# Performance work log

Hardware: AMD Instinct MI355X
Metric: run time of the kernel (lower is better)

Reference implementation:

```python
import jax, jax.numpy as jnp
import numpy as np


def _gcn_layer(x, row, col, W, b):
    # x: [N, d_in]; row/col: [E'] (with self loops already appended)
    N = x.shape[0]
    deg = jax.ops.segment_sum(jnp.ones_like(row, dtype=x.dtype), row, num_segments=N)
    deg_inv_sqrt = deg ** -0.5  # self loops guarantee deg >= 1
    norm = deg_inv_sqrt[row] * deg_inv_sqrt[col]  # [E']
    msg = norm[:, None] * x[row]                  # gather + normalize
    aggr = jax.ops.segment_sum(msg, col, num_segments=N)  # scatter-add
    return aggr @ W + b


def reference(x, edge_index, W1, b1, W2, b2):
    N = x.shape[0]
    loops = jnp.arange(N, dtype=edge_index.dtype)
    row = jnp.concatenate([edge_index[0], loops])
    col = jnp.concatenate([edge_index[1], loops])
    h = jax.nn.relu(_gcn_layer(x, row, col, W1, b1))
    # F.dropout(training=self.training) is identity in eval mode
    out = _gcn_layer(h, row, col, W2, b2)
    return jax.nn.log_softmax(out, axis=1)


def setup_inputs() -> dict:
    key = jax.random.key(0)
    k1, k2, k3, k4 = jax.random.split(key, 4)
    N, E, F_IN, F_HID, F_OUT = 100000, 1200000, 64, 64, 16
    x = jax.random.normal(k1, (N, F_IN), dtype=jnp.float32)
    edge_index = jax.random.randint(k2, (2, E), 0, N, dtype=jnp.int64)
    W1 = jax.random.normal(k3, (F_IN, F_HID), dtype=jnp.float32) / np.sqrt(F_IN)
    b1 = jnp.zeros((F_HID,), dtype=jnp.float32)
    W2 = jax.random.normal(k4, (F_HID, F_OUT), dtype=jnp.float32) / np.sqrt(F_HID)
    b2 = jnp.zeros((F_OUT,), dtype=jnp.float32)
    return {"x": x, "edge_index": edge_index, "W1": W1, "b1": b1, "W2": W2, "b2": b2}
```

## Files before the change

### kernel.cpp

```cpp
#include <hip/hip_runtime.h>
#include <hip/hip_bf16.h>

typedef __attribute__((ext_vector_type(8))) _Float16 hfrag;
typedef __attribute__((ext_vector_type(4))) float ffrag;
typedef __attribute__((ext_vector_type(4))) _Float16 h4v;

#define BSH 8
#define LBS 256
#define CAP_SH 14
#define CAP (1 << CAP_SH)
#define CONV_BLKS 384
#define NF 128
#define NBKP 512

__device__ __forceinline__ float b2f_(unsigned short u) {
    return __uint_as_float(((unsigned)u) << 16);
}
__device__ __forceinline__ unsigned short f2b_(float v) {
    __hip_bfloat16 h = __float2bfloat16(v);
    return *reinterpret_cast<unsigned short*>(&h);
}
__device__ __forceinline__ unsigned short f2h_(float v) {
    _Float16 h = (_Float16)v;
    return __builtin_bit_cast(unsigned short, h);
}
__device__ __forceinline__ float h2f_(unsigned short u) {
    _Float16 h = __builtin_bit_cast(_Float16, u);
    return (float)h;
}

__device__ __forceinline__ float loadF(const void* p, long long i, int isF32) {
    if (isF32) return ((const float*)p)[i];
    return b2f_(((const unsigned short*)p)[i]);
}

__device__ __forceinline__ float4 loadF4(const void* p, long long base, int i4, int isF32) {
    if (isF32) {
        return ((const float4*)((const float*)p + base))[i4];
    } else {
        ushort4 u = ((const ushort4*)((const unsigned short*)p + base))[i4];
        return make_float4(b2f_(u.x), b2f_(u.y), b2f_(u.z), b2f_(u.w));
    }
}

__device__ __forceinline__ void get_edge(const int* ei, int i64, int e, int E, int& s, int& d) {
    if (i64) { s = ei[2 * (long long)e]; d = ei[2 * (long long)E + 2 * (long long)e]; }
    else     { s = ei[e];                d = ei[(long long)E + e]; }
}

struct E4 { int s[4]; int d[4]; };
__device__ __forceinline__ E4 load4(const int* __restrict__ ei, int i64, int e0, int E) {
    E4 r;
    if (i64) {
        const int4* ps = (const int4*)(ei + 2 * (long long)e0);
        const int4* pd = (const int4*)(ei + 2 * (long long)E + 2 * (long long)e0);
        int4 a = ps[0], b = ps[1];
        int4 c = pd[0], d = pd[1];
        r.s[0] = a.x; r.s[1] = a.z; r.s[2] = b.x; r.s[3] = b.z;
        r.d[0] = c.x; r.d[1] = c.z; r.d[2] = d.x; r.d[3] = d.z;
    } else {
        int4 a = *(const int4*)(ei + e0);
        int4 c = *(const int4*)(ei + (long long)E + e0);
        r.s[0] = a.x; r.s[1] = a.y; r.s[2] = a.z; r.s[3] = a.w;
        r.d[0] = c.x; r.d[1] = c.y; r.d[2] = c.z; r.d[3] = c.w;
    }
    return r;
}

__device__ __forceinline__ void wave_scan_excl(int* a, int nEl, int lane) {
    int run = 0;
    for (int base = 0; base < nEl; base += 64) {
        int i = base + lane;
        int orig = (i < nEl) ? a[i] : 0;
        int v = orig;
#pragma unroll
        for (int off = 1; off < 64; off <<= 1) {
            int u = __shfl_up(v, off);
            if (lane >= off) v += u;
        }
        if (i < nEl) a[i] = v - orig + run;
        run += __shfl(v, 63);
    }
}

__global__ void k_prep(const void* x, const int* ei,
                       const void* W1, const void* b1, const void* W2, const void* b2,
                       int* flags, float* Wbuf) {
    __shared__ int s_sane, s_zero;
    int tid = threadIdx.x;
    if (tid == 0) { s_sane = 0; s_zero = 0; }
    __syncthreads();
    const unsigned short* xu = (const unsigned short*)x;
    int sane = 0;
    for (int k = tid; k < 4096; k += 256) {
        float v = b2f_(xu[2 * k]);
        float a = fabsf(v);
        if (v == 0.0f || (a >= 9.3e-10f && a <= 1.1e9f)) sane++;
    }
    if (sane) atomicAdd(&s_sane, sane);
    int zero = 0;
    for (int k = tid; k < 1024; k += 256) if (ei[2 * k + 1] == 0) zero++;
    if (zero) atomicAdd(&s_zero, zero);
    __syncthreads();
    int f = (s_sane < 3000) ? 1 : 0;
    if (tid == 0) { flags[0] = f; flags[1] = (s_zero > 512) ? 1 : 0; }
    for (int i = tid; i < 4096; i += 256) Wbuf[i] = loadF(W1, i, f);
    if (tid < 64) Wbuf[4096 + tid] = loadF(b1, tid, f);
    for (int i = tid; i < 1024; i += 256) Wbuf[4160 + i] = loadF(W2, i, f);
    if (tid < 16) Wbuf[5184 + tid] = loadF(b2, tid, f);
}

__global__ __launch_bounds__(256) void k_s1(const void* __restrict__ x,
                                            const int* __restrict__ ei,
                                            const int* __restrict__ flags,
                                            int E, int N, int nbk,
                                            int* __restrict__ cnt_d, int* __restrict__ cnt_s,
                                            unsigned short* __restrict__ xh) {
    __shared__ int hd[512], hs[512];
    int tid = threadIdx.x;
    if (blockIdx.x < CONV_BLKS) {
        int f = flags[0];
        int n4 = N * 16;
        int ctid = blockIdx.x * 256 + tid;
        int stride = CONV_BLKS * 256 * 2;
        for (int i0 = ctid * 2; i0 < n4; i0 += stride) {
            float4 v0 = loadF4(x, 0, i0, f);
            float4 v1 = (i0 + 1 < n4) ? loadF4(x, 0, i0 + 1, f) : make_float4(0, 0, 0, 0);
            ushort4 o0, o1;
            o0.x = f2h_(v0.x); o0.y = f2h_(v0.y); o0.z = f2h_(v0.z); o0.w = f2h_(v0.w);
            o1.x = f2h_(v1.x); o1.y = f2h_(v1.y); o1.z = f2h_(v1.z); o1.w = f2h_(v1.w);
            ((ushort4*)xh)[i0] = o0;
            if (i0 + 1 < n4) ((ushort4*)xh)[i0 + 1] = o1;
        }
        return;
    }
    for (int i = tid; i < 512; i += 256) { hd[i] = 0; hs[i] = 0; }
    __syncthreads();
    int i64 = flags[1];
    int fb = blockIdx.x - CONV_BLKS;
    int ctid = fb * 256 + tid;
    int stride = NF * 256 * 8;
    for (int e0 = ctid * 8; e0 + 8 <= E; e0 += stride) {
        E4 a = load4(ei, i64, e0, E);
        E4 b = load4(ei, i64, e0 + 4, E);
#pragma unroll
        for (int u = 0; u < 4; ++u) {
            atomicAdd(&hd[a.d[u] >> BSH], 1);
            atomicAdd(&hs[a.s[u] >> BSH], 1);
            atomicAdd(&hd[b.d[u] >> BSH], 1);
            atomicAdd(&hs[b.s[u] >> BSH], 1);
        }
    }
    if (fb == 0 && tid == 0) {
        for (int e = E & ~7; e < E; ++e) {
            int s, d;
            get_edge(ei, i64, e, E, s, d);
            atomicAdd(&hd[d >> BSH], 1);
            atomicAdd(&hs[s >> BSH], 1);
        }
    }
    __syncthreads();
    for (int i = tid; i < nbk; i += 256) {
        cnt_d[fb * NBKP + i] = hd[i];
        cnt_s[fb * NBKP + i] = hs[i];
    }
}

__global__ __launch_bounds__(128) void k_s2(const int* __restrict__ cnt_d,
                                            const int* __restrict__ cnt_s,
                                            int nbk,
                                            int* __restrict__ base_d, int* __restrict__ base_s,
                                            int* __restrict__ td, int* __restrict__ ts) {
    __shared__ int vd[NF], vs[NF];
    __shared__ int lastd, lasts;
    int b = blockIdx.x, tid = threadIdx.x;
    for (int i = tid; i < NF; i += 128) { vd[i] = cnt_d[i * NBKP + b]; vs[i] = cnt_s[i * NBKP + b]; }
    __syncthreads();
    if (tid == 0) lastd = vd[NF - 1];
    if (tid == 1) lasts = vs[NF - 1];
    __syncthreads();
    int lane = tid & 63;
    if (tid < 64)       wave_scan_excl(vd, NF, lane);
    else if (tid < 128) wave_scan_excl(vs, NF, lane);
    __syncthreads();
    for (int i = tid; i < NF; i += 128) {
        base_d[i * NBKP + b] = (b << CAP_SH) + vd[i];
        base_s[i * NBKP + b] = (b << CAP_SH) + vs[i];
    }
    if (tid == 0) td[b] = (b << CAP_SH) + vd[NF - 1] + lastd;
    if (tid == 1) ts[b] = (b << CAP_SH) + vs[NF - 1] + lasts;
}

__global__ __launch_bounds__(256) void k_fill(const int* __restrict__ ei,
                                              const int* __restrict__ flags,
                                              int E, int nbk,
                                              const int* __restrict__ base_d,
                                              const int* __restrict__ base_s,
                                              int* __restrict__ pdst,
                                              unsigned char* __restrict__ psrc) {
    __shared__ int bd[512], bs[512];
    int tid = threadIdx.x;
    int fb = blockIdx.x;
    for (int i = tid; i < nbk; i += 256) {
        bd[i] = base_d[fb * NBKP + i];
        bs[i] = base_s[fb * NBKP + i];
    }
    __syncthreads();
    int i64 = flags[1];
    int ctid = fb * 256 + tid;
    int stride = NF * 256 * 8;
    for (int e0 = ctid * 8; e0 + 8 <= E; e0 += stride) {
        E4 a = load4(ei, i64, e0, E);
        E4 b = load4(ei, i64, e0 + 4, E);
#pragma unroll
        for (int u = 0; u < 4; ++u) {
            int db = a.d[u] >> BSH, sb = a.s[u] >> BSH;
            int p = atomicAdd(&bd[db], 1);
            if (p < ((db + 1) << CAP_SH)) pdst[p] = (a.s[u] << BSH) | (a.d[u] & (LBS - 1));
            int q = atomicAdd(&bs[sb], 1);
            if (q < ((sb + 1) << CAP_SH)) psrc[q] = (unsigned char)(a.s[u] & (LBS - 1));
            db = b.d[u] >> BSH; sb = b.s[u] >> BSH;
            p = atomicAdd(&bd[db], 1);
            if (p < ((db + 1) << CAP_SH)) pdst[p] = (b.s[u] << BSH) | (b.d[u] & (LBS - 1));
            q = atomicAdd(&bs[sb], 1);
            if (q < ((sb + 1) << CAP_SH)) psrc[q] = (unsigned char)(b.s[u] & (LBS - 1));
        }
    }
    if (fb == 0 && tid == 0) {
        for (int e = E & ~7; e < E; ++e) {
            int s, d;
            get_edge(ei, i64, e, E, s, d);
            int db = d >> BSH, sb = s >> BSH;
            int p = atomicAdd(&bd[db], 1);
            if (p < ((db + 1) << CAP_SH)) pdst[p] = (s << BSH) | (d & (LBS - 1));
            int q = atomicAdd(&bs[sb], 1);
            if (q < ((sb + 1) << CAP_SH)) psrc[q] = (unsigned char)(s & (LBS - 1));
        }
    }
}

__global__ __launch_bounds__(256) void k_deg(const unsigned char* __restrict__ psrc,
                                             const int* __restrict__ ts,
                                             float* __restrict__ dis, int N) {
    __shared__ int h[LBS];
    int b = blockIdx.x, tid = threadIdx.x;
    if (tid < LBS) h[tid] = 0;
    __syncthreads();
    int beg = b << CAP_SH;
    int end = min(ts[b], (b + 1) << CAP_SH);
    int cnt = end - beg;
    int nv = cnt & ~3;
    for (int off = 4 * tid; off < nv; off += 1024) {
        uchar4 v = *(const uchar4*)(psrc + beg + off);
        atomicAdd(&h[v.x], 1); atomicAdd(&h[v.y], 1);
        atomicAdd(&h[v.z], 1); atomicAdd(&h[v.w], 1);
    }
    if (tid < cnt - nv) atomicAdd(&h[psrc[beg + nv + tid]], 1);
    __syncthreads();
    if (tid < LBS) {
        int node = b * LBS + tid;
        if (node < N) dis[node] = rsqrtf((float)h[tid] + 1.0f);
    }
}

__global__ __launch_bounds__(256) void k_csr(const int* __restrict__ pdst,
                                             const int* __restrict__ td,
                                             const float* __restrict__ dis,
                                             int2* __restrict__ row_se,
                                             int2* __restrict__ pke, int N) {
    __shared__ int h[LBS], lb[LBS], cur[LBS];
    int b = blockIdx.x, tid = threadIdx.x;
    if (tid < LBS) h[tid] = 0;
    __syncthreads();
    int beg = b << CAP_SH;
    int end = min(td[b], (b + 1) << CAP_SH);
    for (int p = beg + tid; p < end; p += 256) atomicAdd(&h[pdst[p] & (LBS - 1)], 1);
    __syncthreads();
    if (tid < LBS) lb[tid] = h[tid];
    __syncthreads();
    if (tid < 64) wave_scan_excl(lb, LBS, tid);
    __syncthreads();
    if (tid < LBS) {
        cur[tid] = lb[tid];
        int node = b * LBS + tid;
        if (node < N) row_se[node] = make_int2(beg + lb[tid], beg + lb[tid] + h[tid]);
    }
    __syncthreads();
    for (int p = beg + tid; p < end; p += 256) {
        int e = pdst[p];
        int src = e >> BSH, ld = e & (LBS - 1);
        int r = atomicAdd(&cur[ld], 1);
        pke[beg + r] = make_int2(src, __float_as_int(dis[src]));
    }
}

__global__ __launch_bounds__(256) void k_agg(const unsigned short* __restrict__ xh,
                                             const float* __restrict__ dis,
                                             const int2* __restrict__ row_se,
                                             const int2* __restrict__ pke,
                                             unsigned short* __restrict__ aggb, int N) {
    int tid = threadIdx.x;
    int lane = tid & 63;
    int g = lane >> 4, i4 = lane & 15;
    int n = blockIdx.x * 16 + (tid >> 6) * 4 + g;
    if (n >= N) return;
    float dd = dis[n];
    int2 se = row_se[n];
    int beg = se.x, end = se.y;
    int cnt = end - beg;
    h4v xv = *(const h4v*)(xh + (long long)n * 64 + i4 * 4);
    float w = dd * dd;
    float4 A[4];
    A[0].x = w * (float)xv[0]; A[0].y = w * (float)xv[1];
    A[0].z = w * (float)xv[2]; A[0].w = w * (float)xv[3];
#pragma unroll
    for (int u = 1; u < 4; ++u) A[u] = make_float4(0.f, 0.f, 0.f, 0.f);
    int T = (cnt + 3) >> 2;
    int p = beg;
    int2 e[4];
#pragma unroll
    for (int u = 0; u < 4; ++u) e[u] = pke[p + u];
    for (int t = 0; t < T; ++t) {
        h4v hv[4];
#pragma unroll
        for (int u = 0; u < 4; ++u) {
            unsigned ex = min((unsigned)e[u].x, (unsigned)(N - 1));
            hv[u] = *(const h4v*)(xh + (long long)ex * 64 + i4 * 4);
        }
        float nv[4];
#pragma unroll
        for (int u = 0; u < 4; ++u) nv[u] = (p + u < end) ? dd * __int_as_float(e[u].y) : 0.f;
#pragma unroll
        for (int u = 0; u < 4; ++u) e[u] = pke[p + 4 + u];
        p += 4;
#pragma unroll
        for (int u = 0; u < 4; ++u) {
            A[u].x += nv[u] * (float)hv[u][0];
            A[u].y += nv[u] * (float)hv[u][1];
            A[u].z += nv[u] * (float)hv[u][2];
            A[u].w += nv[u] * (float)hv[u][3];
        }
    }
    float4 s;
    s.x = A[0].x + A[1].x + A[2].x + A[3].x;
    s.y = A[0].y + A[1].y + A[2].y + A[3].y;
    s.z = A[0].z + A[1].z + A[2].z + A[3].z;
    s.w = A[0].w + A[1].w + A[2].w + A[3].w;
    ushort4 o;
    o.x = f2h_(s.x); o.y = f2h_(s.y); o.z = f2h_(s.z); o.w = f2h_(s.w);
    *(ushort4*)(aggb + (size_t)n * 64 + i4 * 4) = o;
}

__global__ __launch_bounds__(256) void k_dense(const unsigned short* __restrict__ aggb,
                                               const float* __restrict__ Wbuf,
                                               unsigned short* __restrict__ t2b, int N) {
    __shared__ __align__(16) unsigned short Hs[4][16 * 72];
    int tid = threadIdx.x;
    int lane = tid & 63;
    int w = tid >> 6;
    int m = lane & 15, q = lane >> 4;
    int n0 = blockIdx.x * 64 + w * 16;
    if (n0 >= N) return;

    hfrag Bw1[2][4];
#pragma unroll
    for (int kt = 0; kt < 2; ++kt)
#pragma unroll
        for (int nt = 0; nt < 4; ++nt)
#pragma unroll
            for (int j = 0; j < 8; ++j)
                Bw1[kt][nt][j] = (_Float16)Wbuf[(kt * 32 + q * 8 + j) * 64 + nt * 16 + m];
    hfrag Bw2[2];
#pragma unroll
    for (int kt = 0; kt < 2; ++kt)
#pragma unroll
        for (int j = 0; j < 8; ++j)
            Bw2[kt][j] = (_Float16)Wbuf[4160 + (kt * 32 + q * 8 + j) * 16 + m];
    float b1n[4];
#pragma unroll
    for (int nt = 0; nt < 4; ++nt) b1n[nt] = Wbuf[4096 + nt * 16 + m];

    const unsigned short* arow = aggb + (size_t)(n0 + m) * 64 + q * 8;
    hfrag A0 = *(const hfrag*)(arow);
    hfrag A1 = *(const hfrag*)(arow + 32);

    ffrag acc[4];
#pragma unroll
    for (int nt = 0; nt < 4; ++nt) {
        ffrag z = {0.f, 0.f, 0.f, 0.f};
        z = __builtin_amdgcn_mfma_f32_16x16x32_f16(A0, Bw1[0][nt], z, 0, 0, 0);
        z = __builtin_amdgcn_mfma_f32_16x16x32_f16(A1, Bw1[1][nt], z, 0, 0, 0);
        acc[nt] = z;
    }
    unsigned short* hs = &Hs[w][0];
#pragma unroll
    for (int nt = 0; nt < 4; ++nt)
#pragma unroll
        for (int r = 0; r < 4; ++r) {
            float hv = fmaxf(acc[nt][r] + b1n[nt], 0.0f);
            hs[(q * 4 + r) * 72 + nt * 16 + m] = f2h_(hv);
        }
    const unsigned short* hrow = hs + m * 72 + q * 8;
    hfrag H0 = *(const hfrag*)(hrow);
    hfrag H1 = *(const hfrag*)(hrow + 32);
    ffrag t2 = {0.f, 0.f, 0.f, 0.f};
    t2 = __builtin_amdgcn_mfma_f32_16x16x32_f16(H0, Bw2[0], t2, 0, 0, 0);
    t2 = __builtin_amdgcn_mfma_f32_16x16x32_f16(H1, Bw2[1], t2, 0, 0, 0);
#pragma unroll
    for (int r = 0; r < 4; ++r)
        t2b[(size_t)(n0 + q * 4 + r) * 16 + m] = f2h_(t2[r]);
}

__global__ __launch_bounds__(256) void k_l2(const unsigned short* __restrict__ t2b,
                                            const int* __restrict__ flags,
                                            const float* __restrict__ dis,
                                            const int2* __restrict__ row_se,
                                            const int2* __restrict__ pke,
                                            const float* __restrict__ Wbuf,
                                            void* __restrict__ out, int N) {
    int isF32 = flags[0];
    int tid = threadIdx.x, lane = tid & 63;
    int g = lane >> 4, i = lane & 15;
    int n = blockIdx.x * 16 + (tid >> 6) * 4 + g;
    if (n >= N) return;
    float dd = dis[n];
    int2 se = row_se[n];
    int beg = se.x, end = se.y;
    int cnt = end - beg;
    float A[4];
    A[0] = dd * dd * h2f_(t2b[(size_t)n * 16 + i]);
    A[1] = 0.f; A[2] = 0.f; A[3] = 0.f;
    int T = (cnt + 3) >> 2;
    int p = beg;
    int2 e[4];
#pragma unroll
    for (int u = 0; u < 4; ++u) e[u] = pke[p + u];
    for (int t = 0; t < T; ++t) {
        float r[4];
#pragma unroll
        for (int u = 0; u < 4; ++u) {
            unsigned ex = min((unsigned)e[u].x, (unsigned)(N - 1));
            r[u] = h2f_(t2b[(size_t)ex * 16 + i]);
        }
        float nv[4];
#pragma unroll
        for (int u = 0; u < 4; ++u) nv[u] = (p + u < end) ? dd * __int_as_float(e[u].y) : 0.f;
#pragma unroll
        for (int u = 0; u < 4; ++u) e[u] = pke[p + 4 + u];
        p += 4;
#pragma unroll
        for (int u = 0; u < 4; ++u) A[u] += nv[u] * r[u];
    }
    float a0 = A[0] + A[1] + A[2] + A[3];
    float v = a0 + Wbuf[5184 + i];
    float mx = v;
#pragma unroll
    for (int off = 8; off; off >>= 1) mx = fmaxf(mx, __shfl_xor(mx, off, 16));
    float ex = __expf(v - mx);
    float ss = ex;
#pragma unroll
    for (int off = 8; off; off >>= 1) ss += __shfl_xor(ss, off, 16);
    float r = v - mx - logf(ss);
    size_t oi = (size_t)n * 16 + i;
    if (isF32) ((float*)out)[oi] = r;
    else       ((unsigned short*)out)[oi] = f2b_(r);
}

extern "C" void kernel_launch(void* const* d_in, const int* in_sizes, int n_in,
                              void* d_out, int out_size, void* d_ws, size_t ws_size,
                              hipStream_t stream) {
    const void* x  = d_in[0];
    const int*  ei = (const int*)d_in[1];
    const void* W1 = d_in[2];
    const void* b1 = d_in[3];
    const void* W2 = d_in[4];
    const void* b2 = d_in[5];

    const int N = in_sizes[0] / 64;
    const int E = in_sizes[1] / 2;
    const int nbk = (N + LBS - 1) >> BSH;

    char* p = (char*)d_ws;
#define CARVE(ty, name, bytes) ty name = (ty)p; p += (((size_t)(bytes)) + 63) & ~(size_t)63;
    CARVE(int*,   flags,     16)
    CARVE(float*, Wbuf,      5200 * 4)
    CARVE(float*, dis,       (size_t)N * 4)
    CARVE(int2*,  row_se,    (size_t)N * 8)
    CARVE(int*,   cnt_d,     (size_t)NF * NBKP * 4)
    CARVE(int*,   cnt_s,     (size_t)NF * NBKP * 4)
    CARVE(int*,   base_d,    (size_t)NF * NBKP * 4)
    CARVE(int*,   base_s,    (size_t)NF * NBKP * 4)
    CARVE(int*,   td,        (size_t)nbk * 4)
    CARVE(int*,   ts,        (size_t)nbk * 4)
    CARVE(int*,   pdst,      ((size_t)nbk << CAP_SH) * 4)
    CARVE(unsigned char*, psrc, ((size_t)nbk << CAP_SH))
    CARVE(int2*,  pke,       (((size_t)nbk << CAP_SH) + 64) * 8)
    CARVE(unsigned short*, xh,   (size_t)N * 64 * 2)
    CARVE(unsigned short*, aggb, (size_t)N * 64 * 2)
    CARVE(unsigned short*, t2b,  (size_t)N * 16 * 2)
#undef CARVE

    k_prep<<<1, 256, 0, stream>>>(x, ei, W1, b1, W2, b2, flags, Wbuf);
    k_s1<<<CONV_BLKS + NF, 256, 0, stream>>>(x, ei, flags, E, N, nbk, cnt_d, cnt_s, xh);
    k_s2<<<nbk, 128, 0, stream>>>(cnt_d, cnt_s, nbk, base_d, base_s, td, ts);
    k_fill<<<NF, 256, 0, stream>>>(ei, flags, E, nbk, base_d, base_s, pdst, psrc);
    k_deg<<<nbk, 256, 0, stream>>>(psrc, ts, dis, N);
    k_csr<<<nbk, 256, 0, stream>>>(pdst, td, dis, row_se, pke, N);
    k_agg<<<(N + 15) / 16, 256, 0, stream>>>(xh, dis, row_se, pke, aggb, N);
    k_dense<<<(N + 63) / 64, 256, 0, stream>>>(aggb, Wbuf, t2b, N);
    k_l2<<<(N + 15) / 16, 256, 0, stream>>>(t2b, flags, dis, row_se, pke, Wbuf, d_out, N);
}
```

Measured before the change: 217.0 us.

## Merge prep, histogram and scan kernels; recompute bucket offsets inside fill

Folds the flag-detection and weight-conversion prep kernel into the histogram kernel: each block recomputes the format flags locally instead of reading them from global memory. Removes the separate scan kernel by having each fill block sum the per-block counts itself, with counts stored transposed so they can be read as int4 vectors. Doubles the number of histogram/fill blocks. This drops two kernel launches and their serialization points, at the cost of redundant flag sampling per block and redundant prefix sums in every fill block.

```diff
diff --git a/kernel.cpp b/kernel.cpp
--- a/kernel.cpp
+++ b/kernel.cpp
@@ -9,9 +9,8 @@
 #define LBS 256
 #define CAP_SH 14
 #define CAP (1 << CAP_SH)
+#define NF 256
 #define CONV_BLKS 384
-#define NF 128
-#define NBKP 512
 
 __device__ __forceinline__ float b2f_(unsigned short u) {
     return __uint_as_float(((unsigned)u) << 16);
@@ -83,45 +82,53 @@
     }
 }
 
-__global__ void k_prep(const void* x, const int* ei,
-                       const void* W1, const void* b1, const void* W2, const void* b2,
-                       int* flags, float* Wbuf) {
+__global__ __launch_bounds__(256) void k_hist(const void* __restrict__ x,
+                                              const int* __restrict__ ei,
+                                              const void* __restrict__ W1, const void* __restrict__ b1,
+                                              const void* __restrict__ W2, const void* __restrict__ b2,
+                                              int E, int N, int nbk,
+                                              int* __restrict__ flags, float* __restrict__ Wbuf,
+                                              int* __restrict__ cnt_d, int* __restrict__ cnt_s,
+                                              unsigned short* __restrict__ xh) {
+    __shared__ int hd[512], hs[512];
     __shared__ int s_sane, s_zero;
     int tid = threadIdx.x;
     if (tid == 0) { s_sane = 0; s_zero = 0; }
     __syncthreads();
     const unsigned short* xu = (const unsigned short*)x;
-    int sane = 0;
-    for (int k = tid; k < 4096; k += 256) {
-        float v = b2f_(xu[2 * k]);
-        float a = fabsf(v);
-        if (v == 0.0f || (a >= 9.3e-10f && a <= 1.1e9f)) sane++;
-    }
-    if (sane) atomicAdd(&s_sane, sane);
-    int zero = 0;
-    for (int k = tid; k < 1024; k += 256) if (ei[2 * k + 1] == 0) zero++;
-    if (zero) atomicAdd(&s_zero, zero);
-    __syncthreads();
-    int f = (s_sane < 3000) ? 1 : 0;
-    if (tid == 0) { flags[0] = f; flags[1] = (s_zero > 512) ? 1 : 0; }
-    for (int i = tid; i < 4096; i += 256) Wbuf[i] = loadF(W1, i, f);
-    if (tid < 64) Wbuf[4096 + tid] = loadF(b1, tid, f);
-    for (int i = tid; i < 1024; i += 256) Wbuf[4160 + i] = loadF(W2, i, f);
-    if (tid < 16) Wbuf[5184 + tid] = loadF(b2, tid, f);
-}
-
-__global__ __launch_bounds__(256) void k_s1(const void* __restrict__ x,
-                                            const int* __restrict__ ei,
-                                            const int* __restrict__ flags,
-                                            int E, int N, int nbk,
-                                            int* __restrict__ cnt_d, int* __restrict__ cnt_s,
-                                            unsigned short* __restrict__ xh) {
-    __shared__ int hd[512], hs[512];
-    int tid = threadIdx.x;
-    if (blockIdx.x < CONV_BLKS) {
-        int f = flags[0];
+    if (blockIdx.x == NF) {
+        int sane = 0;
+        for (int k = tid; k < 4096; k += 256) {
+            float v = b2f_(xu[2 * k]);
+            float a = fabsf(v);
+            if (v == 0.0f || (a >= 9.3e-10f && a <= 1.1e9f)) sane++;
+        }
+        if (sane) atomicAdd(&s_sane, sane);
+        int zero = 0;
+        for (int k = tid; k < 1024; k += 256) if (ei[2 * k + 1] == 0) zero++;
+        if (zero) atomicAdd(&s_zero, zero);
+        __syncthreads();
+        int f = (s_sane < 3000) ? 1 : 0;
+        if (tid == 0) { flags[0] = f; flags[1] = (s_zero > 512) ? 1 : 0; }
+        for (int i = tid; i < 4096; i += 256) Wbuf[i] = loadF(W1, i, f);
+        if (tid < 64) Wbuf[4096 + tid] = loadF(b1, tid, f);
+        for (int i = tid; i < 1024; i += 256) Wbuf[4160 + i] = loadF(W2, i, f);
+        if (tid < 16) Wbuf[5184 + tid] = loadF(b2, tid, f);
+        return;
+    }
+    if (blockIdx.x > NF) {
+        int cb = blockIdx.x - NF - 1;
+        int sane = 0;
+        for (int k = tid; k < 4096; k += 256) {
+            float v = b2f_(xu[2 * k]);
+            float a = fabsf(v);
+            if (v == 0.0f || (a >= 9.3e-10f && a <= 1.1e9f)) sane++;
+        }
+        if (sane) atomicAdd(&s_sane, sane);
+        __syncthreads();
+        int f = (s_sane < 3000) ? 1 : 0;
         int n4 = N * 16;
-        int ctid = blockIdx.x * 256 + tid;
+        int ctid = cb * 256 + tid;
         int stride = CONV_BLKS * 256 * 2;
         for (int i0 = ctid * 2; i0 < n4; i0 += stride) {
             float4 v0 = loadF4(x, 0, i0, f);
@@ -134,10 +141,13 @@
         }
         return;
     }
+    int zero = 0;
+    for (int k = tid; k < 1024; k += 256) if (ei[2 * k + 1] == 0) zero++;
+    if (zero) atomicAdd(&s_zero, zero);
     for (int i = tid; i < 512; i += 256) { hd[i] = 0; hs[i] = 0; }
     __syncthreads();
-    int i64 = flags[1];
-    int fb = blockIdx.x - CONV_BLKS;
+    int i64 = (s_zero > 512) ? 1 : 0;
+    int fb = blockIdx.x;
     int ctid = fb * 256 + tid;
     int stride = NF * 256 * 8;
     for (int e0 = ctid * 8; e0 + 8 <= E; e0 += stride) {
@@ -160,53 +170,48 @@
         }
     }
     __syncthreads();
-    for (int i = tid; i < nbk; i += 256) {
-        cnt_d[fb * NBKP + i] = hd[i];
-        cnt_s[fb * NBKP + i] = hs[i];
-    }
-}
-
-__global__ __launch_bounds__(128) void k_s2(const int* __restrict__ cnt_d,
-                                            const int* __restrict__ cnt_s,
-                                            int nbk,
-                                            int* __restrict__ base_d, int* __restrict__ base_s,
-                                            int* __restrict__ td, int* __restrict__ ts) {
-    __shared__ int vd[NF], vs[NF];
-    __shared__ int lastd, lasts;
-    int b = blockIdx.x, tid = threadIdx.x;
-    for (int i = tid; i < NF; i += 128) { vd[i] = cnt_d[i * NBKP + b]; vs[i] = cnt_s[i * NBKP + b]; }
-    __syncthreads();
-    if (tid == 0) lastd = vd[NF - 1];
-    if (tid == 1) lasts = vs[NF - 1];
-    __syncthreads();
-    int lane = tid & 63;
-    if (tid < 64)       wave_scan_excl(vd, NF, lane);
-    else if (tid < 128) wave_scan_excl(vs, NF, lane);
-    __syncthreads();
-    for (int i = tid; i < NF; i += 128) {
-        base_d[i * NBKP + b] = (b << CAP_SH) + vd[i];
-        base_s[i * NBKP + b] = (b << CAP_SH) + vs[i];
-    }
-    if (tid == 0) td[b] = (b << CAP_SH) + vd[NF - 1] + lastd;
-    if (tid == 1) ts[b] = (b << CAP_SH) + vs[NF - 1] + lasts;
+    for (int b = tid; b < nbk; b += 256) {
+        cnt_d[b * NF + fb] = hd[b];
+        cnt_s[b * NF + fb] = hs[b];
+    }
 }
 
 __global__ __launch_bounds__(256) void k_fill(const int* __restrict__ ei,
-                                              const int* __restrict__ flags,
                                               int E, int nbk,
-                                              const int* __restrict__ base_d,
-                                              const int* __restrict__ base_s,
+                                              const int* __restrict__ cnt_d,
+                                              const int* __restrict__ cnt_s,
+                                              int* __restrict__ td, int* __restrict__ ts,
                                               int* __restrict__ pdst,
                                               unsigned char* __restrict__ psrc) {
     __shared__ int bd[512], bs[512];
+    __shared__ int s_zero;
     int tid = threadIdx.x;
+    if (tid == 0) s_zero = 0;
+    __syncthreads();
+    int zero = 0;
+    for (int k = tid; k < 1024; k += 256) if (ei[2 * k + 1] == 0) zero++;
+    if (zero) atomicAdd(&s_zero, zero);
     int fb = blockIdx.x;
-    for (int i = tid; i < nbk; i += 256) {
-        bd[i] = base_d[fb * NBKP + i];
-        bs[i] = base_s[fb * NBKP + i];
-    }
-    __syncthreads();
-    int i64 = flags[1];
+    for (int b = tid; b < nbk; b += 256) {
+        int pre_d = 0, tot_d = 0, pre_s = 0, tot_s = 0;
+        const int* rd = cnt_d + b * NF;
+        const int* rs = cnt_s + b * NF;
+        for (int j = 0; j < NF; j += 4) {
+            int4 vd = *(const int4*)(rd + j);
+            int4 vs = *(const int4*)(rs + j);
+            tot_d += vd.x + vd.y + vd.z + vd.w;
+            tot_s += vs.x + vs.y + vs.z + vs.w;
+            if (j + 0 < fb) { pre_d += vd.x; pre_s += vs.x; }
+            if (j + 1 < fb) { pre_d += vd.y; pre_s += vs.y; }
+            if (j + 2 < fb) { pre_d += vd.z; pre_s += vs.z; }
+            if (j + 3 < fb) { pre_d += vd.w; pre_s += vs.w; }
+        }
+        bd[b] = (b << CAP_SH) + pre_d;
+        bs[b] = (b << CAP_SH) + pre_s;
+        if (fb == 0) { td[b] = (b << CAP_SH) + tot_d; ts[b] = (b << CAP_SH) + tot_s; }
+    }
+    __syncthreads();
+    int i64 = (s_zero > 512) ? 1 : 0;
     int ctid = fb * 256 + tid;
     int stride = NF * 256 * 8;
     for (int e0 = ctid * 8; e0 + 8 <= E; e0 += stride) {
@@ -486,10 +491,8 @@
     CARVE(float*, Wbuf,      5200 * 4)
     CARVE(float*, dis,       (size_t)N * 4)
     CARVE(int2*,  row_se,    (size_t)N * 8)
-    CARVE(int*,   cnt_d,     (size_t)NF * NBKP * 4)
-    CARVE(int*,   cnt_s,     (size_t)NF * NBKP * 4)
-    CARVE(int*,   base_d,    (size_t)NF * NBKP * 4)
-    CARVE(int*,   base_s,    (size_t)NF * NBKP * 4)
+    CARVE(int*,   cnt_d,     (size_t)nbk * NF * 4)
+    CARVE(int*,   cnt_s,     (size_t)nbk * NF * 4)
     CARVE(int*,   td,        (size_t)nbk * 4)
     CARVE(int*,   ts,        (size_t)nbk * 4)
     CARVE(int*,   pdst,      ((size_t)nbk << CAP_SH) * 4)
@@ -500,10 +503,9 @@
     CARVE(unsigned short*, t2b,  (size_t)N * 16 * 2)
 #undef CARVE
 
-    k_prep<<<1, 256, 0, stream>>>(x, ei, W1, b1, W2, b2, flags, Wbuf);
-    k_s1<<<CONV_BLKS + NF, 256, 0, stream>>>(x, ei, flags, E, N, nbk, cnt_d, cnt_s, xh);
-    k_s2<<<nbk, 128, 0, stream>>>(cnt_d, cnt_s, nbk, base_d, base_s, td, ts);
-    k_fill<<<NF, 256, 0, stream>>>(ei, flags, E, nbk, base_d, base_s, pdst, psrc);
+    k_hist<<<NF + 1 + CONV_BLKS, 256, 0, stream>>>(x, ei, W1, b1, W2, b2, E, N, nbk,
+                                                   flags, Wbuf, cnt_d, cnt_s, xh);
+    k_fill<<<NF, 256, 0, stream>>>(ei, E, nbk, cnt_d, cnt_s, td, ts, pdst, psrc);
     k_deg<<<nbk, 256, 0, stream>>>(psrc, ts, dis, N);
     k_csr<<<nbk, 256, 0, stream>>>(pdst, td, dis, row_se, pke, N);
     k_agg<<<(N + 15) / 16, 256, 0, stream>>>(xh, dis, row_se, pke, aggb, N);
```

New measurement: 223.6 us. 3.0% more time.
